# Optimization experiments

Hardware: AMD Instinct MI355X
Metric: run time of the kernel (lower is better)

The kernel has to match this reference:

```python
import jax, jax.numpy as jnp
import numpy as np

N, E, G = 10000, 160000, 64          # nodes, edges, graphs
T, FIN, ED, FOUT = 5, 75, 50, 15     # towers, channels, edge-emb dim, per-tower out
EPS_BN, EPS_STD = 1e-5, 1e-5


def setup_inputs() -> dict:
    key = jax.random.key(0)
    ks = jax.random.split(key, 16)
    s = 0.05
    return dict(
        x=jax.random.randint(ks[0], (N,), 0, 21),
        edge_index=jax.random.randint(ks[1], (2, E), 0, N),
        edge_attr=jax.random.randint(ks[2], (E,), 0, 4),
        batch=jnp.sort(jax.random.randint(ks[3], (N,), 0, G)),
        node_emb=jax.random.normal(ks[4], (21, FIN), dtype=jnp.float32),
        edge_emb=jax.random.normal(ks[5], (4, ED), dtype=jnp.float32),
        We=jax.random.normal(ks[6], (4, ED, FIN), dtype=jnp.float32) * s,
        be=jnp.zeros((4, FIN), jnp.float32),
        Wpre=jax.random.normal(ks[7], (4, T, 3 * FIN, FIN), dtype=jnp.float32) * s,
        bpre=jnp.zeros((4, T, FIN), jnp.float32),
        Wpost=jax.random.normal(ks[8], (4, T, 13 * FIN, FOUT), dtype=jnp.float32) * s,
        bpost=jnp.zeros((4, T, FOUT), jnp.float32),
        Wlin=jax.random.normal(ks[9], (4, FIN, FIN), dtype=jnp.float32) * s,
        blin=jnp.zeros((4, FIN), jnp.float32),
        bn_gamma=jnp.ones((4, FIN), jnp.float32),
        bn_beta=jnp.zeros((4, FIN), jnp.float32),
        uaf=jnp.array([1.1, -0.01, 1e-5, -0.9, 1e-5], dtype=jnp.float32),
        mW1=jax.random.normal(ks[10], (FIN, 50), dtype=jnp.float32) * s,
        mb1=jnp.zeros((50,), jnp.float32),
        mW2=jax.random.normal(ks[11], (50, 25), dtype=jnp.float32) * s,
        mb2=jnp.zeros((25,), jnp.float32),
        mW3=jax.random.normal(ks[12], (25, 1), dtype=jnp.float32) * s,
        mb3=jnp.zeros((1,), jnp.float32),
    )


def _uaf(v, p):
    # softplus(A*(x+B) + C*x^2) - softplus(D*(x-B)) + E
    return (jax.nn.softplus(p[0] * (v + p[1]) + p[2] * v * v)
            - jax.nn.softplus(p[3] * (v - p[1])) + p[4])


def _pna_layer(h, src, dst, e_feat, We, be, Wpre, bpre, Wpost, bpost, Wl, bl,
               deg, avg_log):
    eemb = e_feat @ We + be                      # [E, FIN] edge encoder
    x_i, x_j = h[dst], h[src]                    # [E, FIN] gathers
    # pre-MLP: per-tower Linear(cat[x_i, x_j, e], 3F -> F), split weight blocks
    W1, W2, W3 = Wpre[:, :FIN], Wpre[:, FIN:2 * FIN], Wpre[:, 2 * FIN:]
    m = (jnp.einsum('ec,tcf->etf', x_i, W1)
         + jnp.einsum('ec,tcf->etf', x_j, W2)
         + jnp.einsum('ec,tcf->etf', eemb, W3) + bpre)   # [E, T, FIN]
    degc = jnp.maximum(deg, 1.0)[:, None, None]
    mean = jax.ops.segment_sum(m, dst, N) / degc          # [N, T, FIN]
    mean_sq = jax.ops.segment_sum(m * m, dst, N) / degc
    empty = (deg == 0.0)[:, None, None]
    mn = jnp.where(empty, 0.0, jax.ops.segment_min(m, dst, N))
    mx = jnp.where(empty, 0.0, jax.ops.segment_max(m, dst, N))
    std = jnp.sqrt(jax.nn.relu(mean_sq - mean * mean) + EPS_STD)
    agg = jnp.concatenate([mean, mn, mx, std], axis=-1)   # [N, T, 4F]
    amp = (jnp.log(jnp.maximum(deg, 1.0) + 1.0) / avg_log)[:, None, None]
    out = jnp.concatenate([agg, agg * amp, agg / amp], axis=-1)  # [N, T, 12F]
    # cat tower input (divide_input=False -> full x per tower)
    out = jnp.concatenate(
        [jnp.broadcast_to(h[:, None, :], (N, T, FIN)), out], axis=-1)  # [N,T,13F]
    out = jnp.einsum('ntc,tcf->ntf', out, Wpost) + bpost  # [N, T, FOUT]
    return out.reshape(N, T * FOUT) @ Wl + bl             # [N, FIN]


def reference(node_emb, edge_emb, We, be, Wpre, bpre, Wpost, bpost, Wlin, blin,
              bn_gamma, bn_beta, uaf, mW1, mb1, mW2, mb2, mW3, mb3,
              x, edge_index, edge_attr, batch):
    src, dst = edge_index[0], edge_index[1]
    h = node_emb[x]                              # [N, 75]
    e_feat = edge_emb[edge_attr]                 # [E, 50]
    deg = jax.ops.segment_sum(jnp.ones((E,), h.dtype), dst, N)
    avg_log = jnp.mean(jnp.log(deg + 1.0))       # PNA avg degree (log) statistic
    for l in range(4):
        out = _pna_layer(h, src, dst, e_feat, We[l], be[l], Wpre[l], bpre[l],
                         Wpost[l], bpost[l], Wlin[l], blin[l], deg, avg_log)
        mu = out.mean(axis=0)
        var = out.var(axis=0)                    # biased, training-mode BN
        out = (out - mu) * jax.lax.rsqrt(var + EPS_BN) * bn_gamma[l] + bn_beta[l]
        h = _uaf(out, uaf)
    pooled = jax.ops.segment_sum(h, batch, G)    # global_add_pool -> [G, 75]
    z = _uaf(pooled @ mW1 + mb1, uaf)
    z = _uaf(z @ mW2 + mb2, uaf)
    return z @ mW3 + mb3                         # [G, 1]
```

## Files before the change

### kernel.cpp

```cpp
#include <hip/hip_runtime.h>
#include <hip/hip_fp16.h>
#include <math.h>

static constexpr int N_   = 10000;
static constexpr int E_   = 160000;
static constexpr int G_   = 64;
static constexpr int T_   = 5;
static constexpr int FIN_ = 75;
static constexpr int ED_  = 50;
static constexpr int FOUT_= 15;
static constexpr int TF_  = T_*FIN_;
static constexpr int AGGW_= 4*FIN_;
static constexpr int YC_  = 48;
static constexpr int NP_  = 10112;
static constexpr int AW_  = 400;
static constexpr int BW_  = 384;
static constexpr int WK_  = 380;

__device__ __forceinline__ float softplus_f(float x){
    return fmaxf(x, 0.f) + log1pf(expf(-fabsf(x)));
}
__device__ __forceinline__ float uaf_f(float v, const float* __restrict__ p){
    return softplus_f(p[0]*(v + p[1]) + p[2]*v*v) - softplus_f(p[3]*(v - p[1])) + p[4];
}
__device__ __forceinline__ unsigned pack2h(float a, float b){
    __half2 h = __floats2half2_rn(a, b);
    return *reinterpret_cast<unsigned*>(&h);
}

__global__ void k_h0(const int* __restrict__ x, const float* __restrict__ node_emb, float* __restrict__ hT){
    int i = blockIdx.x*blockDim.x + threadIdx.x;
    if (i >= 80*N_) return;
    int q = i / N_, n = i % N_;
    hT[(size_t)q*NP_ + n] = (q < FIN_) ? node_emb[x[n]*FIN_ + q] : 0.f;
}

__global__ void k_deg(const int* __restrict__ ei, int* __restrict__ deg_i){
    int e = blockIdx.x*blockDim.x + threadIdx.x;
    if (e >= E_) return;
    atomicAdd(&deg_i[ei[E_ + e]], 1);
}

__global__ void k_scan(const int* __restrict__ deg_i, int* __restrict__ offs, float* __restrict__ avglog){
    __shared__ int sd[1024];
    __shared__ float sf[1024];
    __shared__ int carry;
    if (threadIdx.x == 0) carry = 0;
    __syncthreads();
    float ls = 0.f;
    for (int base = 0; base < N_; base += 1024){
        int i = base + threadIdx.x;
        int v = (i < N_) ? deg_i[i] : 0;
        if (i < N_) ls += logf((float)v + 1.f);
        sd[threadIdx.x] = v;
        __syncthreads();
        for (int off = 1; off < 1024; off <<= 1){
            int t = (threadIdx.x >= off) ? sd[threadIdx.x - off] : 0;
            __syncthreads();
            sd[threadIdx.x] += t;
            __syncthreads();
        }
        if (i < N_) offs[i] = carry + sd[threadIdx.x] - v;
        __syncthreads();
        if (threadIdx.x == 0) carry += sd[1023];
        __syncthreads();
    }
    if (threadIdx.x == 0) offs[N_] = carry;
    sf[threadIdx.x] = ls;
    __syncthreads();
    for (int off = 512; off > 0; off >>= 1){
        if (threadIdx.x < off) sf[threadIdx.x] += sf[threadIdx.x + off];
        __syncthreads();
    }
    if (threadIdx.x == 0) avglog[0] = sf[0] / (float)N_;
}

__global__ void k_fill(const int* __restrict__ ei, const int* __restrict__ eattr,
                       const int* __restrict__ offs, int* __restrict__ cursor, int* __restrict__ csr){
    int e = blockIdx.x*blockDim.x + threadIdx.x;
    if (e >= E_) return;
    int d = ei[E_ + e];
    int pos = offs[d] + atomicAdd(&cursor[d], 1);
    csr[pos] = ei[e] | (eattr[e] << 16);
}

__global__ void k_amp(const int* __restrict__ deg_i, const float* __restrict__ avglog,
                      float* __restrict__ ampv, float* __restrict__ iampv){
    int n = blockIdx.x*blockDim.x + threadIdx.x;
    if (n >= N_) return;
    float dm = fmaxf((float)deg_i[n], 1.f);
    float a = logf(dm + 1.f) / avglog[0];
    ampv[n] = a;
    iampv[n] = 1.f / a;
}

__global__ void k_eemb(const float* __restrict__ edge_emb, const float* __restrict__ We,
                       const float* __restrict__ be, float* __restrict__ eembw){
    int i = blockIdx.x*blockDim.x + threadIdx.x;
    if (i >= 4*4*FIN_) return;
    int c = i % FIN_;
    int a = (i / FIN_) % 4;
    int l = i / (4*FIN_);
    float s = be[l*FIN_ + c];
    for (int k = 0; k < ED_; k++) s = fmaf(edge_emb[a*ED_ + k], We[(l*ED_ + k)*FIN_ + c], s);
    eembw[i] = s;
}

__global__ void k_tbl(const float* __restrict__ eembw, const float* __restrict__ Wpre,
                      const float* __restrict__ bpre, float* __restrict__ tbl){
    int i = blockIdx.x*blockDim.x + threadIdx.x;
    if (i >= 4*4*TF_) return;
    int f = i % FIN_;
    int t = (i / FIN_) % T_;
    int a = (i / TF_) % 4;
    int l = i / (4*TF_);
    float s = bpre[(l*T_ + t)*FIN_ + f];
    const float* em = eembw + (l*4 + a)*FIN_;
    const float* W3 = Wpre + ((size_t)(l*T_ + t)*225 + 2*FIN_)*FIN_;
    for (int c = 0; c < FIN_; c++) s = fmaf(em[c], W3[c*FIN_ + f], s);
    tbl[i] = s;
}

__global__ void k_wcomb(const float* __restrict__ Wpost, float* __restrict__ Wcomb){
    int i = blockIdx.x*blockDim.x + threadIdx.x;
    if (i >= 4*T_*WK_*YC_) return;
    int j = i % YC_;
    int c = (i / YC_) % WK_;
    int t = (i / (YC_*WK_)) % T_;
    int l = i / (YC_*WK_*T_);
    float v = 0.f;
    if (j < 45){
        int blk = j / 15, fo = j % 15;
        const float* Wp = Wpost + (size_t)(l*T_ + t)*975*15;
        if (c < FIN_){ if (blk == 0) v = Wp[c*15 + fo]; }
        else if (c >= 80){
            int r = c - 80;
            int fi = r >> 2, kind = r & 3;
            v = Wp[(FIN_ + blk*AGGW_ + kind*FIN_ + fi)*15 + fo];
        }
    }
    Wcomb[i] = v;
}

__global__ void k_wlin80(const float* __restrict__ Wlin, float* __restrict__ Wlin80){
    int i = blockIdx.x*blockDim.x + threadIdx.x;
    if (i >= 4*FIN_*80) return;
    int q = i % 80;
    int p = (i / 80) % FIN_;
    int l = i / (80*FIN_);
    Wlin80[i] = (q < FIN_) ? Wlin[(l*FIN_ + p)*FIN_ + q] : 0.f;
}

__global__ void __launch_bounds__(256) k_A2(const float* __restrict__ hT, const float* __restrict__ Wpre_l,
                                            float* __restrict__ Af, __half* __restrict__ Bh){
    __shared__ float Act[FIN_*128];
    __shared__ float Wt[FIN_*80];
    int chunk = blockIdx.y;
    int t = chunk >> 1, half = chunk & 1;
    const float* __restrict__ W = Wpre_l + (size_t)(t*225 + half*FIN_)*FIN_;
    int n0 = blockIdx.x * 128;
    int tid = threadIdx.x;
    for (int i = tid; i < FIN_*80; i += 256){
        int r = i / 80, c = i - r*80;
        Wt[i] = (c < FIN_) ? W[r*FIN_ + c] : 0.f;
    }
    for (int i = tid; i < FIN_*128; i += 256){
        int r = i >> 7, n = i & 127;
        Act[i] = hT[(size_t)r*NP_ + n0 + n];
    }
    __syncthreads();
    int tn = tid & 31, tj = tid >> 5;
    float acc[4][10];
    #pragma unroll
    for (int m = 0; m < 4; m++)
        #pragma unroll
        for (int j = 0; j < 10; j++) acc[m][j] = 0.f;
    #pragma unroll 5
    for (int k = 0; k < FIN_; k++){
        float4 av = *(const float4*)(Act + (k<<7) + (tn<<2));
        const float* wr = Wt + k*80 + tj*10;
        #pragma unroll
        for (int j = 0; j < 10; j++){
            float wv = wr[j];
            acc[0][j] = fmaf(av.x, wv, acc[0][j]);
            acc[1][j] = fmaf(av.y, wv, acc[1][j]);
            acc[2][j] = fmaf(av.z, wv, acc[2][j]);
            acc[3][j] = fmaf(av.w, wv, acc[3][j]);
        }
    }
    int nodeb = n0 + tn*4;
    #pragma unroll
    for (int m = 0; m < 4; m++){
        int node = nodeb + m;
        if (node >= N_) continue;
        if (half == 0){
            float2* dst = (float2*)(Af + (size_t)node*AW_ + t*80 + tj*10);
            #pragma unroll
            for (int j = 0; j < 5; j++) dst[j] = make_float2(acc[m][2*j], acc[m][2*j+1]);
        } else {
            unsigned* dst = (unsigned*)(Bh + (size_t)node*BW_ + t*76 + tj*10);
            int cnt = (tj == 7) ? 3 : 5;
            for (int j = 0; j < cnt; j++) dst[j] = pack2h(acc[m][2*j], acc[m][2*j+1]);
        }
    }
}

__global__ void __launch_bounds__(128) k_agg(const float* __restrict__ Af, const __half* __restrict__ Bh,
                                             const int* __restrict__ offs, const int* __restrict__ csr,
                                             const float* __restrict__ tbl_l, uint2* __restrict__ agg2h){
    __shared__ float tl[4*TF_];
    int bid = blockIdx.x;
    int n = (bid & 7)*1250 + (bid >> 3);
    for (int idx = threadIdx.x; idx < 4*TF_; idx += 128) tl[idx] = tbl_l[idx];
    __syncthreads();
    int s = offs[n], e_end = offs[n+1];
    int f0 = threadIdx.x;
    int f1 = threadIdx.x + 128;
    int f2r = threadIdx.x + 256;
    int f2 = (f2r < TF_) ? f2r : 0;
    int aoA0 = (f0/FIN_)*80 + f0%FIN_;
    int aoA1 = (f1/FIN_)*80 + f1%FIN_;
    int aoA2 = (f2/FIN_)*80 + f2%FIN_;
    int aoB0 = (f0/FIN_)*76 + f0%FIN_;
    int aoB1 = (f1/FIN_)*76 + f1%FIN_;
    int aoB2 = (f2/FIN_)*76 + f2%FIN_;
    const float* An = Af + (size_t)n*AW_;
    float a0 = An[aoA0], a1 = An[aoA1], a2 = An[aoA2];
    float s0=0.f,s1=0.f,s2=0.f, q0=0.f,q1=0.f,q2=0.f;
    float mn0=INFINITY,mn1=INFINITY,mn2=INFINITY;
    float mx0=-INFINITY,mx1=-INFINITY,mx2=-INFINITY;
    int e = s;
    for (; e + 1 < e_end; e += 2){
        int pk0 = csr[e], pk1 = csr[e+1];
        const __half* B0 = Bh + (size_t)(pk0 & 0xFFFF)*BW_;
        const __half* B1 = Bh + (size_t)(pk1 & 0xFFFF)*BW_;
        const float* t0 = tl + (pk0 >> 16)*TF_;
        const float* t1 = tl + (pk1 >> 16)*TF_;
        float bA0 = __half2float(B0[aoB0]), bA1 = __half2float(B0[aoB1]), bA2 = __half2float(B0[aoB2]);
        float bB0 = __half2float(B1[aoB0]), bB1 = __half2float(B1[aoB1]), bB2 = __half2float(B1[aoB2]);
        float mA0 = a0 + bA0 + t0[f0], mB0 = a0 + bB0 + t1[f0];
        float mA1 = a1 + bA1 + t0[f1], mB1 = a1 + bB1 + t1[f1];
        float mA2 = a2 + bA2 + t0[f2], mB2 = a2 + bB2 + t1[f2];
        s0 += mA0 + mB0; s1 += mA1 + mB1; s2 += mA2 + mB2;
        q0 = fmaf(mA0,mA0,q0); q0 = fmaf(mB0,mB0,q0);
        q1 = fmaf(mA1,mA1,q1); q1 = fmaf(mB1,mB1,q1);
        q2 = fmaf(mA2,mA2,q2); q2 = fmaf(mB2,mB2,q2);
        mn0 = fminf(mn0, fminf(mA0,mB0)); mx0 = fmaxf(mx0, fmaxf(mA0,mB0));
        mn1 = fminf(mn1, fminf(mA1,mB1)); mx1 = fmaxf(mx1, fmaxf(mA1,mB1));
        mn2 = fminf(mn2, fminf(mA2,mB2)); mx2 = fmaxf(mx2, fmaxf(mA2,mB2));
    }
    if (e < e_end){
        int pk0 = csr[e];
        const __half* B0 = Bh + (size_t)(pk0 & 0xFFFF)*BW_;
        const float* t0 = tl + (pk0 >> 16)*TF_;
        float mA0 = a0 + __half2float(B0[aoB0]) + t0[f0];
        float mA1 = a1 + __half2float(B0[aoB1]) + t0[f1];
        float mA2 = a2 + __half2float(B0[aoB2]) + t0[f2];
        s0 += mA0; q0 = fmaf(mA0,mA0,q0); mn0 = fminf(mn0,mA0); mx0 = fmaxf(mx0,mA0);
        s1 += mA1; q1 = fmaf(mA1,mA1,q1); mn1 = fminf(mn1,mA1); mx1 = fmaxf(mx1,mA1);
        s2 += mA2; q2 = fmaf(mA2,mA2,q2); mn2 = fminf(mn2,mA2); mx2 = fmaxf(mx2,mA2);
    }
    float deg = (float)(e_end - s);
    float dc = fmaxf(deg, 1.f);
    float inv = 1.f / dc;
    bool empty = (deg == 0.f);
    {
        float mean = s0*inv;
        float sd = sqrtf(fmaxf(q0*inv - mean*mean, 0.f) + 1e-5f);
        int t = f0/FIN_, fi = f0%FIN_;
        uint2 o; o.x = pack2h(mean, empty?0.f:mn0); o.y = pack2h(empty?0.f:mx0, sd);
        agg2h[(size_t)(t*FIN_+fi)*NP_ + n] = o;
    }
    {
        float mean = s1*inv;
        float sd = sqrtf(fmaxf(q1*inv - mean*mean, 0.f) + 1e-5f);
        int t = f1/FIN_, fi = f1%FIN_;
        uint2 o; o.x = pack2h(mean, empty?0.f:mn1); o.y = pack2h(empty?0.f:mx1, sd);
        agg2h[(size_t)(t*FIN_+fi)*NP_ + n] = o;
    }
    if (f2r < TF_){
        float mean = s2*inv;
        float sd = sqrtf(fmaxf(q2*inv - mean*mean, 0.f) + 1e-5f);
        int t = f2r/FIN_, fi = f2r%FIN_;
        uint2 o; o.x = pack2h(mean, empty?0.f:mn2); o.y = pack2h(empty?0.f:mx2, sd);
        agg2h[(size_t)(t*FIN_+fi)*NP_ + n] = o;
    }
}

__device__ __forceinline__ void unp4(float* Ad, int i, uint2 u){
    int fq = i >> 7, n = i & 127;
    __half2 lo = *reinterpret_cast<__half2*>(&u.x);
    __half2 hi = *reinterpret_cast<__half2*>(&u.y);
    Ad[(fq*4+0)*128 + n] = __low2float(lo);
    Ad[(fq*4+1)*128 + n] = __high2float(lo);
    Ad[(fq*4+2)*128 + n] = __low2float(hi);
    Ad[(fq*4+3)*128 + n] = __high2float(hi);
}

__global__ void __launch_bounds__(256) k_post5(const float* __restrict__ hT, const uint2* __restrict__ agg2h,
                                               const float* __restrict__ Wcomb_l, float* __restrict__ YbT){
    __shared__ float Act[2][20*128];
    __shared__ float Wt[2][20*YC_];
    int t = blockIdx.y;
    int n0 = blockIdx.x * 128;
    int tid = threadIdx.x;
    int tn = tid & 31, tj = tid >> 5;
    const float* __restrict__ Wl = Wcomb_l + (size_t)t*WK_*YC_;
    const uint2* __restrict__ agt = agg2h + (size_t)t*FIN_*NP_;

    for (int i = tid; i < 640; i += 256){
        int r = i >> 5, c4 = i & 31;
        *(float4*)(&Act[0][r*128 + c4*4]) = *(const float4*)(hT + (size_t)r*NP_ + n0 + c4*4);
    }
    if (tid < 240){
        int r = tid / 12, c4 = tid % 12;
        *(float4*)(&Wt[0][r*YC_ + c4*4]) = *(const float4*)(Wl + r*YC_ + c4*4);
    }
    __syncthreads();

    float acc[4][6];
    #pragma unroll
    for (int m = 0; m < 4; m++)
        #pragma unroll
        for (int j = 0; j < 6; j++) acc[m][j] = 0.f;

    float4 pa0, pa1, pa2, pw;
    uint2  pb0, pb1, pb2;
    #pragma unroll 1
    for (int ch = 0; ch < 19; ch++){
        int buf = ch & 1;
        int ch1 = ch + 1;
        bool have = (ch1 < 19);
        bool nh = (ch1 < 4);
        if (have){
            if (nh){
                const float* s = hT + (size_t)(ch1*20)*NP_ + n0;
                { int i0 = tid;       pa0 = *(const float4*)(s + (size_t)(i0 >> 5)*NP_ + (i0 & 31)*4); }
                { int i1 = tid + 256; pa1 = *(const float4*)(s + (size_t)(i1 >> 5)*NP_ + (i1 & 31)*4); }
                if (tid < 128){ int i2 = tid + 512; pa2 = *(const float4*)(s + (size_t)(i2 >> 5)*NP_ + (i2 & 31)*4); }
            } else {
                const uint2* s = agt + (size_t)((ch1 - 4)*5)*NP_ + n0;
                { int i0 = tid;       pb0 = s[(size_t)(i0 >> 7)*NP_ + (i0 & 127)]; }
                { int i1 = tid + 256; pb1 = s[(size_t)(i1 >> 7)*NP_ + (i1 & 127)]; }
                if (tid < 128){ int i2 = tid + 512; pb2 = s[(size_t)(i2 >> 7)*NP_ + (i2 & 127)]; }
            }
            if (tid < 240){
                int r = tid / 12, c4 = tid % 12;
                pw = *(const float4*)(Wl + (size_t)(ch1*20 + r)*YC_ + c4*4);
            }
        }
        const float* A = Act[buf];
        const float* Wb = Wt[buf];
        #pragma unroll
        for (int k = 0; k < 20; k++){
            float4 av = *(const float4*)(A + (k<<7) + (tn<<2));
            const float* wr = Wb + k*YC_ + tj*6;
            #pragma unroll
            for (int j = 0; j < 6; j++){
                float wv = wr[j];
                acc[0][j] = fmaf(av.x, wv, acc[0][j]);
                acc[1][j] = fmaf(av.y, wv, acc[1][j]);
                acc[2][j] = fmaf(av.z, wv, acc[2][j]);
                acc[3][j] = fmaf(av.w, wv, acc[3][j]);
            }
        }
        if (have){
            float* Ad = Act[buf ^ 1];
            float* Wd = Wt[buf ^ 1];
            if (nh){
                { int i0 = tid;       *(float4*)(&Ad[(i0 >> 5)*128 + (i0 & 31)*4]) = pa0; }
                { int i1 = tid + 256; *(float4*)(&Ad[(i1 >> 5)*128 + (i1 & 31)*4]) = pa1; }
                if (tid < 128){ int i2 = tid + 512; *(float4*)(&Ad[(i2 >> 5)*128 + (i2 & 31)*4]) = pa2; }
            } else {
                unp4(Ad, tid, pb0);
                unp4(Ad, tid + 256, pb1);
                if (tid < 128) unp4(Ad, tid + 512, pb2);
            }
            if (tid < 240){ int r = tid / 12, c4 = tid % 12; *(float4*)(&Wd[r*YC_ + c4*4]) = pw; }
            __syncthreads();
        }
    }
    int nodeb = n0 + tn*4;
    #pragma unroll
    for (int j = 0; j < 6; j++){
        int col = t*YC_ + tj*6 + j;
        float4 v = make_float4(acc[0][j], acc[1][j], acc[2][j], acc[3][j]);
        if (nodeb + 3 < N_){
            *(float4*)(YbT + (size_t)col*NP_ + nodeb) = v;
        } else {
            #pragma unroll
            for (int m = 0; m < 4; m++)
                if (nodeb + m < N_) YbT[(size_t)col*NP_ + nodeb + m] = (&v.x)[m];
        }
    }
}

__global__ void __launch_bounds__(64) k_Y(const float* __restrict__ YbT, const float* __restrict__ ampv,
                                          const float* __restrict__ iampv, const float* __restrict__ bpost_l,
                                          const float* __restrict__ Wlin80_l, const float* __restrict__ blin_l,
                                          float* __restrict__ olinT, float* __restrict__ bnsum, float* __restrict__ bnsq){
    __shared__ float st[64*77];
    int qbase = blockIdx.y * 40;
    int qcnt  = blockIdx.y ? 35 : 40;
    int n = blockIdx.x*64 + threadIdx.x;
    int nn = (n < N_) ? n : N_-1;
    bool valid = (n < N_);
    float amp = ampv[nn], iamp = iampv[nn];
    #pragma unroll 1
    for (int t = 0; t < T_; t++){
        #pragma unroll
        for (int fo = 0; fo < FOUT_; fo++){
            float v = YbT[(size_t)(t*YC_ + fo)*NP_ + nn]
                    + amp  * YbT[(size_t)(t*YC_ + 15 + fo)*NP_ + nn]
                    + iamp * YbT[(size_t)(t*YC_ + 30 + fo)*NP_ + nn]
                    + bpost_l[t*FOUT_ + fo];
            st[threadIdx.x*77 + t*FOUT_ + fo] = v;
        }
    }
    __syncthreads();
    float acc[40];
    #pragma unroll
    for (int k = 0; k < 40; k++) acc[k] = (qbase + k < FIN_) ? blin_l[qbase + k] : 0.f;
    #pragma unroll 1
    for (int p = 0; p < FIN_; p++){
        float yv = st[threadIdx.x*77 + p];
        const float* Wp = Wlin80_l + p*80 + qbase;
        #pragma unroll
        for (int k = 0; k < 40; k++) acc[k] = fmaf(yv, Wp[k], acc[k]);
    }
    if (valid){
        #pragma unroll
        for (int k = 0; k < 40; k++){
            int q = qbase + k;
            if (q < FIN_) olinT[(size_t)q*NP_ + n] = acc[k];
        }
    }
    __syncthreads();
    #pragma unroll
    for (int k = 0; k < 40; k++) st[threadIdx.x*77 + k] = valid ? acc[k] : 0.f;
    __syncthreads();
    for (int qq = threadIdx.x; qq < qcnt; qq += 64){
        float s = 0.f, s2 = 0.f;
        #pragma unroll 4
        for (int m = 0; m < 64; m++){ float v = st[m*77 + qq]; s += v; s2 = fmaf(v, v, s2); }
        atomicAdd(&bnsum[qbase + qq], s);
        atomicAdd(&bnsq[qbase + qq], s2);
    }
}

__global__ void k_bn(const float* __restrict__ olinT, const float* __restrict__ bnsum, const float* __restrict__ bnsq,
                     const float* __restrict__ gamma_l, const float* __restrict__ beta_l,
                     const float* __restrict__ uafp, float* __restrict__ hT){
    int i = blockIdx.x*blockDim.x + threadIdx.x;
    if (i >= FIN_*N_) return;
    int q = i / N_, n = i % N_;
    float mu = bnsum[q] * (1.f/(float)N_);
    float var = bnsq[q] * (1.f/(float)N_) - mu*mu;
    float xh = (olinT[(size_t)q*NP_ + n] - mu) * rsqrtf(var + 1e-5f) * gamma_l[q] + beta_l[q];
    hT[(size_t)q*NP_ + n] = uaf_f(xh, uafp);
}

__global__ void __launch_bounds__(256) k_pool2(const float* __restrict__ hT, const int* __restrict__ batch,
                                               float* __restrict__ pooled){
    __shared__ int sb[2];
    int g = blockIdx.x;
    if (threadIdx.x < 2){
        int key = g + threadIdx.x;
        int lo = 0, hi = N_;
        while (lo < hi){ int mid = (lo + hi) >> 1; if (batch[mid] < key) lo = mid + 1; else hi = mid; }
        sb[threadIdx.x] = lo;
    }
    __syncthreads();
    int s = sb[0], e = sb[1];
    int wave = threadIdx.x >> 6, lane = threadIdx.x & 63;
    for (int q = wave; q < FIN_; q += 4){
        float sum = 0.f;
        for (int n = s + lane; n < e; n += 64) sum += hT[(size_t)q*NP_ + n];
        #pragma unroll
        for (int off = 32; off > 0; off >>= 1) sum += __shfl_down(sum, off);
        if (lane == 0) pooled[g*FIN_ + q] = sum;
    }
}

__global__ void __launch_bounds__(64) k_mlp(const float* __restrict__ pooled,
        const float* __restrict__ mW1, const float* __restrict__ mb1,
        const float* __restrict__ mW2, const float* __restrict__ mb2,
        const float* __restrict__ mW3, const float* __restrict__ mb3,
        const float* __restrict__ uafp, float* __restrict__ outp){
    __shared__ float pr[FIN_];
    __shared__ float z1[50];
    __shared__ float z2[25];
    int g = blockIdx.x;
    for (int c = threadIdx.x; c < FIN_; c += 64) pr[c] = pooled[g*FIN_ + c];
    __syncthreads();
    if (threadIdx.x < 50){
        float s = mb1[threadIdx.x];
        for (int c = 0; c < FIN_; c++) s = fmaf(pr[c], mW1[c*50 + threadIdx.x], s);
        z1[threadIdx.x] = uaf_f(s, uafp);
    }
    __syncthreads();
    if (threadIdx.x < 25){
        float s = mb2[threadIdx.x];
        for (int c = 0; c < 50; c++) s = fmaf(z1[c], mW2[c*25 + threadIdx.x], s);
        z2[threadIdx.x] = uaf_f(s, uafp);
    }
    __syncthreads();
    if (threadIdx.x == 0){
        float s = mb3[0];
        for (int c = 0; c < 25; c++) s = fmaf(z2[c], mW3[c], s);
        outp[g] = s;
    }
}

extern "C" void kernel_launch(void* const* d_in, const int* in_sizes, int n_in,
                              void* d_out, int out_size, void* d_ws, size_t ws_size,
                              hipStream_t stream) {
    const int* x         = (const int*)d_in[0];
    const int* ei        = (const int*)d_in[1];
    const int* eattr     = (const int*)d_in[2];
    const int* batch     = (const int*)d_in[3];
    const float* node_emb= (const float*)d_in[4];
    const float* edge_emb= (const float*)d_in[5];
    const float* We      = (const float*)d_in[6];
    const float* be      = (const float*)d_in[7];
    const float* Wpre    = (const float*)d_in[8];
    const float* bpre    = (const float*)d_in[9];
    const float* Wpost   = (const float*)d_in[10];
    const float* bpost   = (const float*)d_in[11];
    const float* Wlin    = (const float*)d_in[12];
    const float* blin    = (const float*)d_in[13];
    const float* bn_gamma= (const float*)d_in[14];
    const float* bn_beta = (const float*)d_in[15];
    const float* uafp    = (const float*)d_in[16];
    const float* mW1     = (const float*)d_in[17];
    const float* mb1     = (const float*)d_in[18];
    const float* mW2     = (const float*)d_in[19];
    const float* mb2     = (const float*)d_in[20];
    const float* mW3     = (const float*)d_in[21];
    const float* mb3     = (const float*)d_in[22];
    float* outp          = (float*)d_out;

    char* w = (char*)d_ws;
    auto alloc = [&](size_t bytes) -> void* {
        void* p = (void*)w;
        w += (bytes + 255) & ~(size_t)255;
        return p;
    };
    float*  hT    = (float*)alloc((size_t)80*NP_*4);
    float*  Af    = (float*)alloc((size_t)N_*AW_*4);
    __half* Bh    = (__half*)alloc((size_t)N_*BW_*2);
    uint2*  agg2h = (uint2*)alloc((size_t)TF_*NP_*8);
    float*  YbT   = Af;
    float*  olinT = Af + 3000000;
    float*  ampv  = (float*)alloc(N_*4);
    float*  iampv = (float*)alloc(N_*4);
    float*  avglog= (float*)alloc(4);
    float*  tbl   = (float*)alloc(4*4*TF_*4);
    float*  eembw = (float*)alloc(4*4*FIN_*4);
    float*  Wcomb = (float*)alloc((size_t)4*T_*WK_*YC_*4);
    float*  Wlin80= (float*)alloc(4*FIN_*80*4);
    float*  bnsum = (float*)alloc(2*FIN_*4);
    float*  bnsq  = bnsum + FIN_;
    float*  pooled= (float*)alloc(G_*FIN_*4);
    int* deg_i   = (int*)alloc(N_*4);
    int* offs    = (int*)alloc((N_+1)*4);
    int* cursor  = (int*)alloc(N_*4);
    int* csr     = (int*)alloc(E_*4);

    hipMemsetAsync(deg_i, 0, N_*4, stream);
    hipMemsetAsync(cursor, 0, N_*4, stream);

    k_h0<<<(80*N_ + 255)/256, 256, 0, stream>>>(x, node_emb, hT);
    k_deg<<<(E_ + 255)/256, 256, 0, stream>>>(ei, deg_i);
    k_scan<<<1, 1024, 0, stream>>>(deg_i, offs, avglog);
    k_fill<<<(E_ + 255)/256, 256, 0, stream>>>(ei, eattr, offs, cursor, csr);
    k_amp<<<(N_ + 255)/256, 256, 0, stream>>>(deg_i, avglog, ampv, iampv);
    k_eemb<<<(4*4*FIN_ + 255)/256, 256, 0, stream>>>(edge_emb, We, be, eembw);
    k_tbl<<<(4*4*TF_ + 255)/256, 256, 0, stream>>>(eembw, Wpre, bpre, tbl);
    k_wcomb<<<(4*T_*WK_*YC_ + 255)/256, 256, 0, stream>>>(Wpost, Wcomb);
    k_wlin80<<<(4*FIN_*80 + 255)/256, 256, 0, stream>>>(Wlin, Wlin80);

    int nmb = (N_ + 127)/128;
    int nrb = (N_ + 63)/64;
    for (int l = 0; l < 4; l++){
        hipMemsetAsync(bnsum, 0, 2*FIN_*4, stream);
        k_A2<<<dim3(nmb, 10), 256, 0, stream>>>(hT, Wpre + (size_t)l*T_*225*FIN_, Af, Bh);
        k_agg<<<N_, 128, 0, stream>>>(Af, Bh, offs, csr, tbl + (size_t)l*4*TF_, agg2h);
        k_post5<<<dim3(nmb, T_), 256, 0, stream>>>(hT, agg2h, Wcomb + (size_t)l*T_*WK_*YC_, YbT);
        k_Y<<<dim3(nrb, 2), 64, 0, stream>>>(YbT, ampv, iampv, bpost + l*T_*FOUT_,
                                             Wlin80 + (size_t)l*FIN_*80, blin + l*FIN_,
                                             olinT, bnsum, bnsq);
        k_bn<<<(FIN_*N_ + 255)/256, 256, 0, stream>>>(olinT, bnsum, bnsq,
                                                      bn_gamma + l*FIN_, bn_beta + l*FIN_, uafp, hT);
    }

    k_pool2<<<G_, 256, 0, stream>>>(hT, batch, pooled);
    k_mlp<<<G_, 64, 0, stream>>>(pooled, mW1, mb1, mW2, mb2, mW3, mb3, uafp, outp);
}
```

Before: 1.034 ms.

## Split post-MLP GEMM over K into two partial buffers and widen aggregation unroll

The post-aggregation GEMM kernel now uses 64-node tiles with 128 threads and splits the 19 K-chunks into two halves via a third grid dimension. Each half writes its own partial output buffer, and k_Y sums the two partials. This raises the block count to fill more CUs, at the cost of extra global traffic for a second partial buffer and new workspace allocations. The edge aggregation loop is also unrolled by 4 with all gathers issued first, to expose more memory-level parallelism.

New measurement: 932.1 us. 9.9% less time.

```diff
diff --git a/kernel.cpp b/kernel.cpp
--- a/kernel.cpp
+++ b/kernel.cpp
@@ -230,35 +230,40 @@
     float mn0=INFINITY,mn1=INFINITY,mn2=INFINITY;
     float mx0=-INFINITY,mx1=-INFINITY,mx2=-INFINITY;
     int e = s;
-    for (; e + 1 < e_end; e += 2){
-        int pk0 = csr[e], pk1 = csr[e+1];
-        const __half* B0 = Bh + (size_t)(pk0 & 0xFFFF)*BW_;
-        const __half* B1 = Bh + (size_t)(pk1 & 0xFFFF)*BW_;
-        const float* t0 = tl + (pk0 >> 16)*TF_;
-        const float* t1 = tl + (pk1 >> 16)*TF_;
-        float bA0 = __half2float(B0[aoB0]), bA1 = __half2float(B0[aoB1]), bA2 = __half2float(B0[aoB2]);
-        float bB0 = __half2float(B1[aoB0]), bB1 = __half2float(B1[aoB1]), bB2 = __half2float(B1[aoB2]);
-        float mA0 = a0 + bA0 + t0[f0], mB0 = a0 + bB0 + t1[f0];
-        float mA1 = a1 + bA1 + t0[f1], mB1 = a1 + bB1 + t1[f1];
-        float mA2 = a2 + bA2 + t0[f2], mB2 = a2 + bB2 + t1[f2];
-        s0 += mA0 + mB0; s1 += mA1 + mB1; s2 += mA2 + mB2;
-        q0 = fmaf(mA0,mA0,q0); q0 = fmaf(mB0,mB0,q0);
-        q1 = fmaf(mA1,mA1,q1); q1 = fmaf(mB1,mB1,q1);
-        q2 = fmaf(mA2,mA2,q2); q2 = fmaf(mB2,mB2,q2);
-        mn0 = fminf(mn0, fminf(mA0,mB0)); mx0 = fmaxf(mx0, fmaxf(mA0,mB0));
-        mn1 = fminf(mn1, fminf(mA1,mB1)); mx1 = fmaxf(mx1, fmaxf(mA1,mB1));
-        mn2 = fminf(mn2, fminf(mA2,mB2)); mx2 = fmaxf(mx2, fmaxf(mA2,mB2));
-    }
-    if (e < e_end){
-        int pk0 = csr[e];
-        const __half* B0 = Bh + (size_t)(pk0 & 0xFFFF)*BW_;
-        const float* t0 = tl + (pk0 >> 16)*TF_;
-        float mA0 = a0 + __half2float(B0[aoB0]) + t0[f0];
-        float mA1 = a1 + __half2float(B0[aoB1]) + t0[f1];
-        float mA2 = a2 + __half2float(B0[aoB2]) + t0[f2];
-        s0 += mA0; q0 = fmaf(mA0,mA0,q0); mn0 = fminf(mn0,mA0); mx0 = fmaxf(mx0,mA0);
-        s1 += mA1; q1 = fmaf(mA1,mA1,q1); mn1 = fminf(mn1,mA1); mx1 = fmaxf(mx1,mA1);
-        s2 += mA2; q2 = fmaf(mA2,mA2,q2); mn2 = fminf(mn2,mA2); mx2 = fmaxf(mx2,mA2);
+    for (; e + 3 < e_end; e += 4){
+        float b0[4], b1[4], b2[4];
+        const float* tt[4];
+        #pragma unroll
+        for (int u = 0; u < 4; u++){
+            int pk = csr[e + u];
+            const __half* B = Bh + (size_t)(pk & 0xFFFF)*BW_;
+            tt[u] = tl + (pk >> 16)*TF_;
+            b0[u] = __half2float(B[aoB0]);
+            b1[u] = __half2float(B[aoB1]);
+            b2[u] = __half2float(B[aoB2]);
+        }
+        #pragma unroll
+        for (int u = 0; u < 4; u++){
+            float m0 = a0 + b0[u] + tt[u][f0];
+            float m1 = a1 + b1[u] + tt[u][f1];
+            float m2 = a2 + b2[u] + tt[u][f2];
+            s0 += m0; s1 += m1; s2 += m2;
+            q0 = fmaf(m0,m0,q0); q1 = fmaf(m1,m1,q1); q2 = fmaf(m2,m2,q2);
+            mn0 = fminf(mn0,m0); mx0 = fmaxf(mx0,m0);
+            mn1 = fminf(mn1,m1); mx1 = fmaxf(mx1,m1);
+            mn2 = fminf(mn2,m2); mx2 = fmaxf(mx2,m2);
+        }
+    }
+    for (; e < e_end; e++){
+        int pk = csr[e];
+        const __half* B = Bh + (size_t)(pk & 0xFFFF)*BW_;
+        const float* t0 = tl + (pk >> 16)*TF_;
+        float m0 = a0 + __half2float(B[aoB0]) + t0[f0];
+        float m1 = a1 + __half2float(B[aoB1]) + t0[f1];
+        float m2 = a2 + __half2float(B[aoB2]) + t0[f2];
+        s0 += m0; q0 = fmaf(m0,m0,q0); mn0 = fminf(mn0,m0); mx0 = fmaxf(mx0,m0);
+        s1 += m1; q1 = fmaf(m1,m1,q1); mn1 = fminf(mn1,m1); mx1 = fmaxf(mx1,m1);
+        s2 += m2; q2 = fmaf(m2,m2,q2); mn2 = fminf(mn2,m2); mx2 = fmaxf(mx2,m2);
     }
     float deg = (float)(e_end - s);
     float dc = fmaxf(deg, 1.f);
@@ -287,34 +292,46 @@
     }
 }
 
-__device__ __forceinline__ void unp4(float* Ad, int i, uint2 u){
-    int fq = i >> 7, n = i & 127;
+__device__ __forceinline__ void unp4_64(float* Ad, int i, uint2 u){
+    int fq = i >> 6, n = i & 63;
     __half2 lo = *reinterpret_cast<__half2*>(&u.x);
     __half2 hi = *reinterpret_cast<__half2*>(&u.y);
-    Ad[(fq*4+0)*128 + n] = __low2float(lo);
-    Ad[(fq*4+1)*128 + n] = __high2float(lo);
-    Ad[(fq*4+2)*128 + n] = __low2float(hi);
-    Ad[(fq*4+3)*128 + n] = __high2float(hi);
-}
-
-__global__ void __launch_bounds__(256) k_post5(const float* __restrict__ hT, const uint2* __restrict__ agg2h,
-                                               const float* __restrict__ Wcomb_l, float* __restrict__ YbT){
-    __shared__ float Act[2][20*128];
+    Ad[(fq*4+0)*64 + n] = __low2float(lo);
+    Ad[(fq*4+1)*64 + n] = __high2float(lo);
+    Ad[(fq*4+2)*64 + n] = __low2float(hi);
+    Ad[(fq*4+3)*64 + n] = __high2float(hi);
+}
+
+__global__ void __launch_bounds__(128) k_post6(const float* __restrict__ hT, const uint2* __restrict__ agg2h,
+                                               const float* __restrict__ Wcomb_l,
+                                               float* __restrict__ Yp0, float* __restrict__ Yp1){
+    __shared__ float Act[2][20*64];
     __shared__ float Wt[2][20*YC_];
     int t = blockIdx.y;
-    int n0 = blockIdx.x * 128;
+    int kz = blockIdx.z;
+    int c0 = kz ? 9 : 0;
+    int c1 = kz ? 19 : 9;
+    float* __restrict__ Yp = kz ? Yp1 : Yp0;
+    int n0 = blockIdx.x * 64;
     int tid = threadIdx.x;
-    int tn = tid & 31, tj = tid >> 5;
+    int tn = tid & 15, tj = tid >> 4;
     const float* __restrict__ Wl = Wcomb_l + (size_t)t*WK_*YC_;
     const uint2* __restrict__ agt = agg2h + (size_t)t*FIN_*NP_;
 
-    for (int i = tid; i < 640; i += 256){
-        int r = i >> 5, c4 = i & 31;
-        *(float4*)(&Act[0][r*128 + c4*4]) = *(const float4*)(hT + (size_t)r*NP_ + n0 + c4*4);
-    }
-    if (tid < 240){
-        int r = tid / 12, c4 = tid % 12;
-        *(float4*)(&Wt[0][r*YC_ + c4*4]) = *(const float4*)(Wl + r*YC_ + c4*4);
+    if (c0 < 4){
+        const float* sp = hT + (size_t)(c0*20)*NP_ + n0;
+        for (int i = tid; i < 320; i += 128){
+            int r = i >> 4, c4 = i & 15;
+            *(float4*)(&Act[0][r*64 + c4*4]) = *(const float4*)(sp + (size_t)r*NP_ + c4*4);
+        }
+    } else {
+        const uint2* sp = agt + (size_t)((c0 - 4)*5)*NP_ + n0;
+        for (int i = tid; i < 320; i += 128)
+            unp4_64(Act[0], i, sp[(size_t)(i >> 6)*NP_ + (i & 63)]);
+    }
+    for (int i = tid; i < 240; i += 128){
+        int r = i / 12, c4 = i % 12;
+        *(float4*)(&Wt[0][r*YC_ + c4*4]) = *(const float4*)(Wl + (size_t)(c0*20 + r)*YC_ + c4*4);
     }
     __syncthreads();
 
@@ -324,36 +341,36 @@
         #pragma unroll
         for (int j = 0; j < 6; j++) acc[m][j] = 0.f;
 
-    float4 pa0, pa1, pa2, pw;
+    float4 ph0, ph1, ph2, pw0, pw1;
     uint2  pb0, pb1, pb2;
     #pragma unroll 1
-    for (int ch = 0; ch < 19; ch++){
-        int buf = ch & 1;
+    for (int ch = c0; ch < c1; ch++){
+        int buf = (ch - c0) & 1;
         int ch1 = ch + 1;
-        bool have = (ch1 < 19);
+        bool have = (ch1 < c1);
         bool nh = (ch1 < 4);
         if (have){
             if (nh){
-                const float* s = hT + (size_t)(ch1*20)*NP_ + n0;
-                { int i0 = tid;       pa0 = *(const float4*)(s + (size_t)(i0 >> 5)*NP_ + (i0 & 31)*4); }
-                { int i1 = tid + 256; pa1 = *(const float4*)(s + (size_t)(i1 >> 5)*NP_ + (i1 & 31)*4); }
-                if (tid < 128){ int i2 = tid + 512; pa2 = *(const float4*)(s + (size_t)(i2 >> 5)*NP_ + (i2 & 31)*4); }
+                const float* sp = hT + (size_t)(ch1*20)*NP_ + n0;
+                { int i0 = tid;       ph0 = *(const float4*)(sp + (size_t)(i0 >> 4)*NP_ + (i0 & 15)*4); }
+                { int i1 = tid + 128; ph1 = *(const float4*)(sp + (size_t)(i1 >> 4)*NP_ + (i1 & 15)*4); }
+                if (tid < 64){ int i2 = tid + 256; ph2 = *(const float4*)(sp + (size_t)(i2 >> 4)*NP_ + (i2 & 15)*4); }
             } else {
-                const uint2* s = agt + (size_t)((ch1 - 4)*5)*NP_ + n0;
-                { int i0 = tid;       pb0 = s[(size_t)(i0 >> 7)*NP_ + (i0 & 127)]; }
-                { int i1 = tid + 256; pb1 = s[(size_t)(i1 >> 7)*NP_ + (i1 & 127)]; }
-                if (tid < 128){ int i2 = tid + 512; pb2 = s[(size_t)(i2 >> 7)*NP_ + (i2 & 127)]; }
+                const uint2* sp = agt + (size_t)((ch1 - 4)*5)*NP_ + n0;
+                { int i0 = tid;       pb0 = sp[(size_t)(i0 >> 6)*NP_ + (i0 & 63)]; }
+                { int i1 = tid + 128; pb1 = sp[(size_t)(i1 >> 6)*NP_ + (i1 & 63)]; }
+                if (tid < 64){ int i2 = tid + 256; pb2 = sp[(size_t)(i2 >> 6)*NP_ + (i2 & 63)]; }
             }
-            if (tid < 240){
-                int r = tid / 12, c4 = tid % 12;
-                pw = *(const float4*)(Wl + (size_t)(ch1*20 + r)*YC_ + c4*4);
-            }
+            { int i = tid; int r = i / 12, c4 = i % 12;
+              pw0 = *(const float4*)(Wl + (size_t)(ch1*20 + r)*YC_ + c4*4); }
+            if (tid < 112){ int i = tid + 128; int r = i / 12, c4 = i % 12;
+              pw1 = *(const float4*)(Wl + (size_t)(ch1*20 + r)*YC_ + c4*4); }
         }
         const float* A = Act[buf];
         const float* Wb = Wt[buf];
         #pragma unroll
         for (int k = 0; k < 20; k++){
-            float4 av = *(const float4*)(A + (k<<7) + (tn<<2));
+            float4 av = *(const float4*)(A + (k<<6) + (tn<<2));
             const float* wr = Wb + k*YC_ + tj*6;
             #pragma unroll
             for (int j = 0; j < 6; j++){
@@ -368,15 +385,16 @@
             float* Ad = Act[buf ^ 1];
             float* Wd = Wt[buf ^ 1];
             if (nh){
-                { int i0 = tid;       *(float4*)(&Ad[(i0 >> 5)*128 + (i0 & 31)*4]) = pa0; }
-                { int i1 = tid + 256; *(float4*)(&Ad[(i1 >> 5)*128 + (i1 & 31)*4]) = pa1; }
-                if (tid < 128){ int i2 = tid + 512; *(float4*)(&Ad[(i2 >> 5)*128 + (i2 & 31)*4]) = pa2; }
+                { int i0 = tid;       *(float4*)(&Ad[(i0 >> 4)*64 + (i0 & 15)*4]) = ph0; }
+                { int i1 = tid + 128; *(float4*)(&Ad[(i1 >> 4)*64 + (i1 & 15)*4]) = ph1; }
+                if (tid < 64){ int i2 = tid + 256; *(float4*)(&Ad[(i2 >> 4)*64 + (i2 & 15)*4]) = ph2; }
             } else {
-                unp4(Ad, tid, pb0);
-                unp4(Ad, tid + 256, pb1);
-                if (tid < 128) unp4(Ad, tid + 512, pb2);
+                unp4_64(Ad, tid, pb0);
+                unp4_64(Ad, tid + 128, pb1);
+                if (tid < 64) unp4_64(Ad, tid + 256, pb2);
             }
-            if (tid < 240){ int r = tid / 12, c4 = tid % 12; *(float4*)(&Wd[r*YC_ + c4*4]) = pw; }
+            { int i = tid; int r = i / 12, c4 = i % 12; *(float4*)(&Wd[r*YC_ + c4*4]) = pw0; }
+            if (tid < 112){ int i = tid + 128; int r = i / 12, c4 = i % 12; *(float4*)(&Wd[r*YC_ + c4*4]) = pw1; }
             __syncthreads();
         }
     }
@@ -386,16 +404,17 @@
         int col = t*YC_ + tj*6 + j;
         float4 v = make_float4(acc[0][j], acc[1][j], acc[2][j], acc[3][j]);
         if (nodeb + 3 < N_){
-            *(float4*)(YbT + (size_t)col*NP_ + nodeb) = v;
+            *(float4*)(Yp + (size_t)col*NP_ + nodeb) = v;
         } else {
             #pragma unroll
             for (int m = 0; m < 4; m++)
-                if (nodeb + m < N_) YbT[(size_t)col*NP_ + nodeb + m] = (&v.x)[m];
-        }
-    }
-}
-
-__global__ void __launch_bounds__(64) k_Y(const float* __restrict__ YbT, const float* __restrict__ ampv,
+                if (nodeb + m < N_) Yp[(size_t)col*NP_ + nodeb + m] = (&v.x)[m];
+        }
+    }
+}
+
+__global__ void __launch_bounds__(64) k_Y(const float* __restrict__ Yp0, const float* __restrict__ Yp1,
+                                          const float* __restrict__ ampv,
                                           const float* __restrict__ iampv, const float* __restrict__ bpost_l,
                                           const float* __restrict__ Wlin80_l, const float* __restrict__ blin_l,
                                           float* __restrict__ olinT, float* __restrict__ bnsum, float* __restrict__ bnsq){
@@ -410,9 +429,12 @@
     for (int t = 0; t < T_; t++){
         #pragma unroll
         for (int fo = 0; fo < FOUT_; fo++){
-            float v = YbT[(size_t)(t*YC_ + fo)*NP_ + nn]
-                    + amp  * YbT[(size_t)(t*YC_ + 15 + fo)*NP_ + nn]
-                    + iamp * YbT[(size_t)(t*YC_ + 30 + fo)*NP_ + nn]
+            size_t b0 = (size_t)(t*YC_ + fo)*NP_ + nn;
+            size_t b1 = (size_t)(t*YC_ + 15 + fo)*NP_ + nn;
+            size_t b2 = (size_t)(t*YC_ + 30 + fo)*NP_ + nn;
+            float v = (Yp0[b0] + Yp1[b0])
+                    + amp  * (Yp0[b1] + Yp1[b1])
+                    + iamp * (Yp0[b2] + Yp1[b2])
                     + bpost_l[t*FOUT_ + fo];
             st[threadIdx.x*77 + t*FOUT_ + fo] = v;
         }
@@ -550,8 +572,9 @@
     float*  Af    = (float*)alloc((size_t)N_*AW_*4);
     __half* Bh    = (__half*)alloc((size_t)N_*BW_*2);
     uint2*  agg2h = (uint2*)alloc((size_t)TF_*NP_*8);
-    float*  YbT   = Af;
-    float*  olinT = Af + 3000000;
+    float*  Yp0   = (float*)alloc((size_t)T_*YC_*NP_*4);
+    float*  Yp1   = (float*)alloc((size_t)T_*YC_*NP_*4);
+    float*  olinT = (float*)alloc((size_t)FIN_*NP_*4);
     float*  ampv  = (float*)alloc(N_*4);
     float*  iampv = (float*)alloc(N_*4);
     float*  avglog= (float*)alloc(4);
@@ -581,13 +604,13 @@
     k_wlin80<<<(4*FIN_*80 + 255)/256, 256, 0, stream>>>(Wlin, Wlin80);
 
     int nmb = (N_ + 127)/128;
-    int nrb = (N_ + 63)/64;
+    int npb = (N_ + 63)/64;
     for (int l = 0; l < 4; l++){
         hipMemsetAsync(bnsum, 0, 2*FIN_*4, stream);
         k_A2<<<dim3(nmb, 10), 256, 0, stream>>>(hT, Wpre + (size_t)l*T_*225*FIN_, Af, Bh);
         k_agg<<<N_, 128, 0, stream>>>(Af, Bh, offs, csr, tbl + (size_t)l*4*TF_, agg2h);
-        k_post5<<<dim3(nmb, T_), 256, 0, stream>>>(hT, agg2h, Wcomb + (size_t)l*T_*WK_*YC_, YbT);
-        k_Y<<<dim3(nrb, 2), 64, 0, stream>>>(YbT, ampv, iampv, bpost + l*T_*FOUT_,
+        k_post6<<<dim3(npb, T_, 2), 128, 0, stream>>>(hT, agg2h, Wcomb + (size_t)l*T_*WK_*YC_, Yp0, Yp1);
+        k_Y<<<dim3(npb, 2), 64, 0, stream>>>(Yp0, Yp1, ampv, iampv, bpost + l*T_*FOUT_,
                                              Wlin80 + (size_t)l*FIN_*80, blin + l*FIN_,
                                              olinT, bnsum, bnsq);
         k_bn<<<(FIN_*N_ + 255)/256, 256, 0, stream>>>(olinT, bnsum, bnsq,
```
